# Performance work log

Hardware: AMD Instinct MI355X
Metric: run time of the kernel (lower is better)

## Reference

```python
import jax, jax.numpy as jnp
import numpy as np

M, K, N = 8192, 4096, 4096
INT8_MAX = 127.0


def setup_inputs() -> dict:
    key = jax.random.key(0)
    k1, k2, k3, k4 = jax.random.split(key, 4)
    inp = jax.random.normal(k1, (M, K), dtype=jnp.float32)
    # int8 weight [out_features, in_features]
    weight = jax.random.randint(k2, (N, K), -128, 128, dtype=jnp.int32).astype(jnp.int8)
    # per-output-channel dequant scale
    weight_scale = jax.random.uniform(k3, (N,), dtype=jnp.float32, minval=1e-3, maxval=1e-2)
    bias = jax.random.normal(k4, (N,), dtype=jnp.float32) * 0.01
    return {"input": inp, "weight": weight, "weight_scale": weight_scale, "bias": bias}


def reference(input, weight, weight_scale, bias):
    # Dynamic per-token symmetric int8 quantization (scaled_int8_quant with
    # scale=None, azp=None, symmetric=True): scale_a = max|x| / 127 per row.
    absmax = jnp.max(jnp.abs(input), axis=-1, keepdims=True)  # [M, 1]
    scale_a = jnp.where(absmax > 0, absmax / INT8_MAX, jnp.float32(1.0))
    q = jnp.clip(jnp.round(input / scale_a), -128, 127).astype(jnp.int8)  # [M, K]
    # and per-column (weight_scale) dequant, plus bias, in input dtype.
    acc = jnp.matmul(q.astype(jnp.int32), weight.T.astype(jnp.int32))  # [M, N] int32
    out = acc.astype(jnp.float32) * scale_a * weight_scale[None, :] + bias[None, :]
    return out.astype(input.dtype)
```

## Files before the change

### kernel.cpp

```cpp
#include <hip/hip_runtime.h>
#include <cstdint>

typedef __attribute__((ext_vector_type(4))) int int32x4;
typedef __attribute__((ext_vector_type(16))) int int32x16;

#define GLOBAL_AS __attribute__((address_space(1)))
#define LDS_AS    __attribute__((address_space(3)))

__global__ __launch_bounds__(256) void pack_w(
    const int* __restrict__ w32, uint32_t* __restrict__ w8_as_u32)
{
    const size_t i = (size_t)blockIdx.x * 256 + threadIdx.x;
    const int4 v = ((const int4*)w32)[i];
    w8_as_u32[i] = (v.x & 0xff) | ((v.y & 0xff) << 8) |
                   ((v.z & 0xff) << 16) | ((uint32_t)(v.w & 0xff) << 24);
}

__global__ __launch_bounds__(256) void quant_rows(
    const float* __restrict__ in, int8_t* __restrict__ q,
    float* __restrict__ sa, int K)
{
    const int row = blockIdx.x;
    const float4* rp = (const float4*)(in + (size_t)row * K);
    const int t = threadIdx.x;

    float amax = 0.f;
    float4 v[4];
#pragma unroll
    for (int i = 0; i < 4; ++i) {
        v[i] = rp[t + (i << 8)];
        amax = fmaxf(amax,
               fmaxf(fmaxf(fabsf(v[i].x), fabsf(v[i].y)),
                     fmaxf(fabsf(v[i].z), fabsf(v[i].w))));
    }

#pragma unroll
    for (int off = 32; off; off >>= 1)
        amax = fmaxf(amax, __shfl_xor(amax, off));
    __shared__ float smax[4];
    if ((t & 63) == 0) smax[t >> 6] = amax;
    __syncthreads();
    amax = fmaxf(fmaxf(smax[0], smax[1]), fmaxf(smax[2], smax[3]));

    const float scale = (amax > 0.f) ? (amax / 127.f) : 1.f;
    if (t == 0) sa[row] = scale;
    const float rs = 1.f / scale;

    int* qrow = (int*)(q + (size_t)row * K);
#pragma unroll
    for (int i = 0; i < 4; ++i) {
        int a = __float2int_rn(v[i].x * rs);
        int b = __float2int_rn(v[i].y * rs);
        int c = __float2int_rn(v[i].z * rs);
        int d = __float2int_rn(v[i].w * rs);
        a = max(-128, min(127, a));
        b = max(-128, min(127, b));
        c = max(-128, min(127, c));
        d = max(-128, min(127, d));
        qrow[t + (i << 8)] = (a & 0xff) | ((b & 0xff) << 8) |
                             ((c & 0xff) << 16) | ((d & 0xff) << 24);
    }
}

__device__ __forceinline__ void async_load16(const int8_t* g, int8_t* lds) {
    __builtin_amdgcn_global_load_lds((const GLOBAL_AS char*)g,
                                     (LDS_AS char*)lds, 16, 0, 0);
}

__global__ __launch_bounds__(512, 2) void w8a8_gemm(
    const int8_t* __restrict__ Aq, const int8_t* __restrict__ W,
    const float* __restrict__ sa, const float* __restrict__ wsc,
    const float* __restrict__ bias, float* __restrict__ out,
    int M, int N, int K)
{
    __shared__ int8_t lds[4 * 32768];

    const int NB = N >> 8;
    const int nwg = gridDim.x;
    const int cpx = nwg >> 3;
    const int wg = (blockIdx.x & 7) * cpx + (blockIdx.x >> 3);
    const int bm = wg / NB, bn = wg % NB;

    const int t = threadIdx.x;
    const int lane = t & 63, wid = t >> 6;
    const int wr = wid >> 2, wc = wid & 3;
    const int l31 = lane & 31, h = lane >> 5;
    const int pswz = ((lane >> 1) ^ (lane >> 3)) & 3;

    const int srow = t >> 2;
    const int scol = (((t & 3) ^ ((t >> 3) & 3) ^ ((t >> 5) & 3)) << 4);
    const int8_t* gA = Aq + ((size_t)bm * 256 + srow) * (size_t)K + scol;
    const int8_t* gB = W  + ((size_t)bn * 256 + srow) * (size_t)K + scol;
    const size_t half_stride = (size_t)128 * K;
    int8_t* ldsw = &lds[t * 16];

    auto stage = [&](int ring, int kbyte, int c) {
        const int8_t* src = (c < 2 ? gA : gB) + (size_t)(c & 1) * half_stride + kbyte;
        async_load16(src, ldsw + ring * 32768 + (c >> 1) * 16384 + (c & 1) * 8192);
    };

    const int arow = (wr * 128 + l31) * 64;
    const int brow = 16384 + (wc * 64 + l31) * 64;
    const int cs0 = ((0 + h) ^ pswz) << 4;
    const int cs1 = ((2 + h) ^ pswz) << 4;

    int32x16 acc[4][2];
#pragma unroll
    for (int m = 0; m < 4; ++m)
#pragma unroll
        for (int n = 0; n < 2; ++n)
#pragma unroll
            for (int rgi = 0; rgi < 16; ++rgi)
                acc[m][n][rgi] = 0;

    const int NT = K >> 6;

#pragma unroll
    for (int c = 0; c < 4; ++c) stage(0, 0, c);
#pragma unroll
    for (int c = 0; c < 4; ++c) stage(1, 64, c);
    asm volatile("s_waitcnt vmcnt(4)" ::: "memory");
    asm volatile("s_barrier" ::: "memory");

    for (int g = 0; g < NT; ++g) {
        const int rbase = (g & 3) * 32768;
        const int sring = (g + 2) & 3;
        const int skb = (g + 2) << 6;
        const bool do_stage = (g + 2) < NT;
#pragma unroll
        for (int kk = 0; kk < 2; ++kk) {
            const int cs = kk ? cs1 : cs0;

            int32x4 af[4], bf[2];
#pragma unroll
            for (int m = 0; m < 4; ++m)
                af[m] = *(const int32x4*)&lds[rbase + arow + m * 2048 + cs];
#pragma unroll
            for (int n = 0; n < 2; ++n)
                bf[n] = *(const int32x4*)&lds[rbase + brow + n * 2048 + cs];

            if (do_stage) {
                stage(sring, skb, 2 * kk);
                stage(sring, skb, 2 * kk + 1);
            }

            asm volatile("s_barrier" ::: "memory");
            __builtin_amdgcn_s_setprio(1);
#pragma unroll
            for (int m = 0; m < 4; ++m)
#pragma unroll
                for (int n = 0; n < 2; ++n)
                    acc[m][n] = __builtin_amdgcn_mfma_i32_32x32x32_i8(
                        af[m], bf[n], acc[m][n], 0, 0, 0);
            __builtin_amdgcn_s_setprio(0);

            if (kk == 1) {
                if (g < NT - 2)
                    asm volatile("s_waitcnt vmcnt(4)" ::: "memory");
                else
                    asm volatile("s_waitcnt vmcnt(0)" ::: "memory");
            }
            asm volatile("s_barrier" ::: "memory");
        }
    }

    const int col0 = bn * 256 + wc * 64 + l31;
    const int row00 = bm * 256 + wr * 128 + 4 * h;

#pragma unroll
    for (int m = 0; m < 4; ++m) {
        float sv[16];
#pragma unroll
        for (int rgi = 0; rgi < 16; ++rgi)
            sv[rgi] = sa[row00 + m * 32 + (rgi & 3) + 8 * (rgi >> 2)];
#pragma unroll
        for (int n = 0; n < 2; ++n) {
            const int col = col0 + n * 32;
            const float wn = wsc[col];
            const float bb = bias[col];
#pragma unroll
            for (int rgi = 0; rgi < 16; ++rgi) {
                const int row = row00 + m * 32 + (rgi & 3) + 8 * (rgi >> 2);
                out[(size_t)row * N + col] =
                    (float)acc[m][n][rgi] * sv[rgi] * wn + bb;
            }
        }
    }
}

extern "C" void kernel_launch(void* const* d_in, const int* in_sizes, int n_in,
                              void* d_out, int out_size, void* d_ws, size_t ws_size,
                              hipStream_t stream) {
    const float* inp  = (const float*)d_in[0];
    const int*   w32  = (const int*)d_in[1];
    const float* wsc  = (const float*)d_in[2];
    const float* bias = (const float*)d_in[3];
    float* out = (float*)d_out;

    const int N = in_sizes[2];
    const int K = in_sizes[1] / N;
    const int M = in_sizes[0] / K;

    int8_t* q  = (int8_t*)d_ws;
    float*  sa = (float*)((char*)d_ws + (size_t)M * K);
    int8_t* w8 = (int8_t*)((char*)d_ws + (size_t)M * K + (size_t)M * 4 + 256);

    const size_t nw4 = ((size_t)N * K) / 4;
    pack_w<<<(int)(nw4 / 256), 256, 0, stream>>>(w32, (uint32_t*)w8);

    quant_rows<<<M, 256, 0, stream>>>(inp, q, sa, K);

    const int nwg = (M / 256) * (N / 256);
    w8a8_gemm<<<nwg, 512, 0, stream>>>(q, w8, sa, wsc, bias, out, M, N, K);
}
```

Baseline: 199.8 us.

## Use 4-wave workgroups with 128x128 per-wave tiles and single barrier per k-step

Halves the workgroup to 256 threads (4 waves, 2x2), so each wave computes a 128x128 output tile with 4x4 MFMA accumulators instead of 4x2. Each thread now issues two async loads per stage chunk to fill the same 256x256 LDS tile. The two inner k-substeps are merged into one iteration with a single barrier, reading both k-halves' fragments up front. This increases register reuse of A/B fragments and cuts barrier count, at the cost of more accumulator registers per wave (256 VGPRs of acc), one workgroup per CU, and fewer waves to hide latency.

```diff
diff --git a/kernel.cpp b/kernel.cpp
--- a/kernel.cpp
+++ b/kernel.cpp
@@ -67,7 +67,7 @@
                                      (LDS_AS char*)lds, 16, 0, 0);
 }
 
-__global__ __launch_bounds__(512, 2) void w8a8_gemm(
+__global__ __launch_bounds__(256, 1) void w8a8_gemm(
     const int8_t* __restrict__ Aq, const int8_t* __restrict__ W,
     const float* __restrict__ sa, const float* __restrict__ wsc,
     const float* __restrict__ bias, float* __restrict__ out,
@@ -83,7 +83,7 @@
 
     const int t = threadIdx.x;
     const int lane = t & 63, wid = t >> 6;
-    const int wr = wid >> 2, wc = wid & 3;
+    const int wr = wid >> 1, wc = wid & 1;
     const int l31 = lane & 31, h = lane >> 5;
     const int pswz = ((lane >> 1) ^ (lane >> 3)) & 3;
 
@@ -91,24 +91,27 @@
     const int scol = (((t & 3) ^ ((t >> 3) & 3) ^ ((t >> 5) & 3)) << 4);
     const int8_t* gA = Aq + ((size_t)bm * 256 + srow) * (size_t)K + scol;
     const int8_t* gB = W  + ((size_t)bn * 256 + srow) * (size_t)K + scol;
-    const size_t half_stride = (size_t)128 * K;
+    const size_t rstep = (size_t)64 * K;
+    const size_t hstep = (size_t)128 * K;
     int8_t* ldsw = &lds[t * 16];
 
     auto stage = [&](int ring, int kbyte, int c) {
-        const int8_t* src = (c < 2 ? gA : gB) + (size_t)(c & 1) * half_stride + kbyte;
-        async_load16(src, ldsw + ring * 32768 + (c >> 1) * 16384 + (c & 1) * 8192);
+        const int8_t* s0 = (c < 2 ? gA : gB) + (size_t)(c & 1) * hstep + kbyte;
+        int8_t* d0 = ldsw + ring * 32768 + (c >> 1) * 16384 + (c & 1) * 8192;
+        async_load16(s0, d0);
+        async_load16(s0 + rstep, d0 + 4096);
     };
 
-    const int arow = (wr * 128 + l31) * 64;
-    const int brow = 16384 + (wc * 64 + l31) * 64;
+    const int aoff = wr * 8192 + l31 * 64;
+    const int boff = 16384 + wc * 8192 + l31 * 64;
     const int cs0 = ((0 + h) ^ pswz) << 4;
     const int cs1 = ((2 + h) ^ pswz) << 4;
 
-    int32x16 acc[4][2];
+    int32x16 acc[4][4];
 #pragma unroll
     for (int m = 0; m < 4; ++m)
 #pragma unroll
-        for (int n = 0; n < 2; ++n)
+        for (int n = 0; n < 4; ++n)
 #pragma unroll
             for (int rgi = 0; rgi < 16; ++rgi)
                 acc[m][n][rgi] = 0;
@@ -119,7 +122,7 @@
     for (int c = 0; c < 4; ++c) stage(0, 0, c);
 #pragma unroll
     for (int c = 0; c < 4; ++c) stage(1, 64, c);
-    asm volatile("s_waitcnt vmcnt(4)" ::: "memory");
+    asm volatile("s_waitcnt vmcnt(8)" ::: "memory");
     asm volatile("s_barrier" ::: "memory");
 
     for (int g = 0; g < NT; ++g) {
@@ -127,44 +130,48 @@
         const int sring = (g + 2) & 3;
         const int skb = (g + 2) << 6;
         const bool do_stage = (g + 2) < NT;
-#pragma unroll
-        for (int kk = 0; kk < 2; ++kk) {
-            const int cs = kk ? cs1 : cs0;
-
-            int32x4 af[4], bf[2];
-#pragma unroll
-            for (int m = 0; m < 4; ++m)
-                af[m] = *(const int32x4*)&lds[rbase + arow + m * 2048 + cs];
-#pragma unroll
-            for (int n = 0; n < 2; ++n)
-                bf[n] = *(const int32x4*)&lds[rbase + brow + n * 2048 + cs];
-
-            if (do_stage) {
-                stage(sring, skb, 2 * kk);
-                stage(sring, skb, 2 * kk + 1);
-            }
-
-            asm volatile("s_barrier" ::: "memory");
-            __builtin_amdgcn_s_setprio(1);
-#pragma unroll
-            for (int m = 0; m < 4; ++m)
-#pragma unroll
-                for (int n = 0; n < 2; ++n)
-                    acc[m][n] = __builtin_amdgcn_mfma_i32_32x32x32_i8(
-                        af[m], bf[n], acc[m][n], 0, 0, 0);
-            __builtin_amdgcn_s_setprio(0);
-
-            if (kk == 1) {
-                if (g < NT - 2)
-                    asm volatile("s_waitcnt vmcnt(4)" ::: "memory");
-                else
-                    asm volatile("s_waitcnt vmcnt(0)" ::: "memory");
-            }
-            asm volatile("s_barrier" ::: "memory");
+
+        int32x4 a0[4], b0[4], a1[4], b1[4];
+#pragma unroll
+        for (int m = 0; m < 4; ++m)
+            a0[m] = *(const int32x4*)&lds[rbase + aoff + m * 2048 + cs0];
+#pragma unroll
+        for (int n = 0; n < 4; ++n)
+            b0[n] = *(const int32x4*)&lds[rbase + boff + n * 2048 + cs0];
+
+        if (do_stage) {
+#pragma unroll
+            for (int c = 0; c < 4; ++c) stage(sring, skb, c);
         }
-    }
-
-    const int col0 = bn * 256 + wc * 64 + l31;
+
+#pragma unroll
+        for (int m = 0; m < 4; ++m)
+            a1[m] = *(const int32x4*)&lds[rbase + aoff + m * 2048 + cs1];
+#pragma unroll
+        for (int n = 0; n < 4; ++n)
+            b1[n] = *(const int32x4*)&lds[rbase + boff + n * 2048 + cs1];
+
+#pragma unroll
+        for (int m = 0; m < 4; ++m)
+#pragma unroll
+            for (int n = 0; n < 4; ++n)
+                acc[m][n] = __builtin_amdgcn_mfma_i32_32x32x32_i8(
+                    a0[m], b0[n], acc[m][n], 0, 0, 0);
+#pragma unroll
+        for (int m = 0; m < 4; ++m)
+#pragma unroll
+            for (int n = 0; n < 4; ++n)
+                acc[m][n] = __builtin_amdgcn_mfma_i32_32x32x32_i8(
+                    a1[m], b1[n], acc[m][n], 0, 0, 0);
+
+        if (g < NT - 2)
+            asm volatile("s_waitcnt vmcnt(8)" ::: "memory");
+        else
+            asm volatile("s_waitcnt vmcnt(0)" ::: "memory");
+        asm volatile("s_barrier" ::: "memory");
+    }
+
+    const int col0 = bn * 256 + wc * 128 + l31;
     const int row00 = bm * 256 + wr * 128 + 4 * h;
 
 #pragma unroll
@@ -174,7 +181,7 @@
         for (int rgi = 0; rgi < 16; ++rgi)
             sv[rgi] = sa[row00 + m * 32 + (rgi & 3) + 8 * (rgi >> 2)];
 #pragma unroll
-        for (int n = 0; n < 2; ++n) {
+        for (int n = 0; n < 4; ++n) {
             const int col = col0 + n * 32;
             const float wn = wsc[col];
             const float bb = bias[col];
@@ -211,5 +218,5 @@
     quant_rows<<<M, 256, 0, stream>>>(inp, q, sa, K);
 
     const int nwg = (M / 256) * (N / 256);
-    w8a8_gemm<<<nwg, 512, 0, stream>>>(q, w8, sa, wsc, bias, out, M, N, K);
-}
+    w8a8_gemm<<<nwg, 256, 0, stream>>>(q, w8, sa, wsc, bias, out, M, N, K);
+}
```

After: 195.7 us. -2.0%, faster.

## Use fragment-ordered LDS layout and merge k-halves into one barrier per tile

Applied to the files above, without the earlier changes.

Changes the global-to-LDS staging map so each 16-byte chunk lands in the LDS position a lane reads directly as an MFMA fragment. This drops the XOR swizzle and makes fragment reads contiguous per wave, which should avoid bank conflicts. The two k-subiterations are merged so each tile has a single barrier instead of four, with all eight fragments loaded up front. The cost is higher register pressure and global loads where consecutive threads read different rows.

```diff
diff --git a/kernel.cpp b/kernel.cpp
--- a/kernel.cpp
+++ b/kernel.cpp
@@ -85,24 +85,26 @@
     const int lane = t & 63, wid = t >> 6;
     const int wr = wid >> 2, wc = wid & 3;
     const int l31 = lane & 31, h = lane >> 5;
-    const int pswz = ((lane >> 1) ^ (lane >> 3)) & 3;
-
-    const int srow = t >> 2;
-    const int scol = (((t & 3) ^ ((t >> 3) & 3) ^ ((t >> 5) & 3)) << 4);
+
+    const int srow = ((t >> 7) & 3) * 32 + (t & 31);
+    const int scol = ((t >> 5) & 3) << 4;
     const int8_t* gA = Aq + ((size_t)bm * 256 + srow) * (size_t)K + scol;
     const int8_t* gB = W  + ((size_t)bn * 256 + srow) * (size_t)K + scol;
-    const size_t half_stride = (size_t)128 * K;
+    const size_t hstep = (size_t)128 * K;
     int8_t* ldsw = &lds[t * 16];
 
-    auto stage = [&](int ring, int kbyte, int c) {
-        const int8_t* src = (c < 2 ? gA : gB) + (size_t)(c & 1) * half_stride + kbyte;
-        async_load16(src, ldsw + ring * 32768 + (c >> 1) * 16384 + (c & 1) * 8192);
+    auto stage_tile = [&](int slot, int kbyte) {
+        const int8_t* sA = gA + kbyte;
+        const int8_t* sB = gB + kbyte;
+        int8_t* d = ldsw + slot * 32768;
+        async_load16(sA, d);
+        async_load16(sA + hstep, d + 8192);
+        async_load16(sB, d + 16384);
+        async_load16(sB + hstep, d + 16384 + 8192);
     };
 
-    const int arow = (wr * 128 + l31) * 64;
-    const int brow = 16384 + (wc * 64 + l31) * 64;
-    const int cs0 = ((0 + h) ^ pswz) << 4;
-    const int cs1 = ((2 + h) ^ pswz) << 4;
+    const int aoff0 = wr * 8192 + lane * 16;
+    const int boff0 = 16384 + wc * 4096 + lane * 16;
 
     int32x16 acc[4][2];
 #pragma unroll
@@ -115,53 +117,52 @@
 
     const int NT = K >> 6;
 
-#pragma unroll
-    for (int c = 0; c < 4; ++c) stage(0, 0, c);
-#pragma unroll
-    for (int c = 0; c < 4; ++c) stage(1, 64, c);
+    stage_tile(0, 0);
+    stage_tile(1, 64);
     asm volatile("s_waitcnt vmcnt(4)" ::: "memory");
     asm volatile("s_barrier" ::: "memory");
 
     for (int g = 0; g < NT; ++g) {
         const int rbase = (g & 3) * 32768;
-        const int sring = (g + 2) & 3;
-        const int skb = (g + 2) << 6;
         const bool do_stage = (g + 2) < NT;
-#pragma unroll
-        for (int kk = 0; kk < 2; ++kk) {
-            const int cs = kk ? cs1 : cs0;
-
-            int32x4 af[4], bf[2];
-#pragma unroll
-            for (int m = 0; m < 4; ++m)
-                af[m] = *(const int32x4*)&lds[rbase + arow + m * 2048 + cs];
+
+        int32x4 a0[4], b0[2], a1[4], b1[2];
+#pragma unroll
+        for (int m = 0; m < 4; ++m)
+            a0[m] = *(const int32x4*)&lds[rbase + aoff0 + m * 2048];
+#pragma unroll
+        for (int n = 0; n < 2; ++n)
+            b0[n] = *(const int32x4*)&lds[rbase + boff0 + n * 2048];
+
+        if (do_stage) stage_tile((g + 2) & 3, (g + 2) << 6);
+
+#pragma unroll
+        for (int m = 0; m < 4; ++m)
+            a1[m] = *(const int32x4*)&lds[rbase + aoff0 + m * 2048 + 1024];
+#pragma unroll
+        for (int n = 0; n < 2; ++n)
+            b1[n] = *(const int32x4*)&lds[rbase + boff0 + n * 2048 + 1024];
+
+        __builtin_amdgcn_s_setprio(1);
+#pragma unroll
+        for (int m = 0; m < 4; ++m)
 #pragma unroll
             for (int n = 0; n < 2; ++n)
-                bf[n] = *(const int32x4*)&lds[rbase + brow + n * 2048 + cs];
-
-            if (do_stage) {
-                stage(sring, skb, 2 * kk);
-                stage(sring, skb, 2 * kk + 1);
-            }
-
-            asm volatile("s_barrier" ::: "memory");
-            __builtin_amdgcn_s_setprio(1);
-#pragma unroll
-            for (int m = 0; m < 4; ++m)
-#pragma unroll
-                for (int n = 0; n < 2; ++n)
-                    acc[m][n] = __builtin_amdgcn_mfma_i32_32x32x32_i8(
-                        af[m], bf[n], acc[m][n], 0, 0, 0);
-            __builtin_amdgcn_s_setprio(0);
-
-            if (kk == 1) {
-                if (g < NT - 2)
-                    asm volatile("s_waitcnt vmcnt(4)" ::: "memory");
-                else
-                    asm volatile("s_waitcnt vmcnt(0)" ::: "memory");
-            }
-            asm volatile("s_barrier" ::: "memory");
-        }
+                acc[m][n] = __builtin_amdgcn_mfma_i32_32x32x32_i8(
+                    a0[m], b0[n], acc[m][n], 0, 0, 0);
+#pragma unroll
+        for (int m = 0; m < 4; ++m)
+#pragma unroll
+            for (int n = 0; n < 2; ++n)
+                acc[m][n] = __builtin_amdgcn_mfma_i32_32x32x32_i8(
+                    a1[m], b1[n], acc[m][n], 0, 0, 0);
+        __builtin_amdgcn_s_setprio(0);
+
+        if (g < NT - 2)
+            asm volatile("s_waitcnt vmcnt(4)" ::: "memory");
+        else
+            asm volatile("s_waitcnt vmcnt(0)" ::: "memory");
+        asm volatile("s_barrier" ::: "memory");
     }
 
     const int col0 = bn * 256 + wc * 64 + l31;
```

Result: slower. 206.9 us (+3.6%).
